# Kernel optimization log

Measured on AMD Instinct MI355X. Metric: run time of the kernel, lower is better.

The kernel has to match this reference:

```python
import jax, jax.numpy as jnp
import numpy as np

OUT, IN = 4096, 4096
PACKED = (OUT * IN + 1) // 2


def setup_inputs() -> dict:
    key = jax.random.key(0)
    k1, k2, k3, k4, k5 = jax.random.split(key, 5)
    x = jax.random.normal(k1, (4, 2048, IN), dtype=jnp.float32)
    weight_packed = jax.random.randint(k2, (PACKED,), 0, 256, dtype=jnp.int32)
    scale = jax.random.uniform(k3, (OUT, 1), dtype=jnp.float32) * 0.01 + 1e-4
    zero_point = jax.random.uniform(k4, (OUT, 1), dtype=jnp.float32) * 8.0
    bias = jax.random.normal(k5, (OUT,), dtype=jnp.float32) * 0.02
    return {"x": x, "weight_packed": weight_packed, "scale": scale,
            "zero_point": zero_point, "bias": bias}


def _dequant_weight(weight_packed, scale, zero_point):
    # Unpack two 4-bit nibbles per byte; low nibble first (matches torch.stack dim=1 + flatten)
    low = (weight_packed & 15).astype(jnp.float32)          # [PACKED]
    high = ((weight_packed >> 4) & 15).astype(jnp.float32)   # [PACKED]
    unpacked = jnp.stack([low, high], axis=1).reshape(-1)     # [2*PACKED]
    w = unpacked[: OUT * IN].reshape(OUT, IN)
    # weight * scale - zero_point * scale == (weight - zero_point) * scale
    return (w - zero_point) * scale                           # [OUT, IN]


def reference(x, weight_packed, scale, zero_point, bias):
    w = _dequant_weight(weight_packed, scale, zero_point)
    # F.linear: x @ w.T + bias
    return jnp.einsum('bsi,oi->bso', x, w) + bias
```

## Files before the change

kernel.cpp:

```cpp
#include <hip/hip_runtime.h>
#include <hip/hip_bf16.h>


typedef __bf16 bf16;
typedef __attribute__((ext_vector_type(8))) __bf16 bf16x8;
typedef __attribute__((ext_vector_type(4))) float f32x4;
typedef __attribute__((ext_vector_type(4))) unsigned int u32x4;

#define OUT_DIM 4096
#define IN_DIM  4096
#define M_DIM   8192

__global__ __launch_bounds__(256) void cvt_x_kernel(
    const float* __restrict__ x, bf16* __restrict__ xb)
{
  const long t = (long)blockIdx.x * 256 + threadIdx.x;
  const long i = t * 8;
  const f32x4 a = *(const f32x4*)(x + i);
  const f32x4 b = *(const f32x4*)(x + i + 4);
  union { bf16 h[8]; u32x4 u; } r;
#pragma unroll
  for (int q = 0; q < 4; ++q) { r.h[q] = (bf16)a[q]; r.h[4+q] = (bf16)b[q]; }
  *(u32x4*)(xb + i) = r.u;
}

__global__ __launch_bounds__(256) void repack_w_kernel(
    const int* __restrict__ wp, unsigned int* __restrict__ wb)
{
  const long t = (long)blockIdx.x * 256 + threadIdx.x;
  const long e = t * 16;
  u32x4 r;
#pragma unroll
  for (int q = 0; q < 4; ++q) {
    const int4 p = *(const int4*)(wp + e + q * 4);
    r[q] = (unsigned)(p.x & 255) | ((unsigned)(p.y & 255) << 8) |
           ((unsigned)(p.z & 255) << 16) | ((unsigned)(p.w & 255) << 24);
  }
  *(u32x4*)(wb + t * 4) = r;
}

__global__ __launch_bounds__(512, 2) void gemm_bt_bias_kernel(
    const bf16* __restrict__ A, const unsigned char* __restrict__ WP,
    const float* __restrict__ scale, const float* __restrict__ zp,
    const float* __restrict__ bias, float* __restrict__ C)
{
  const int N = OUT_DIM, K = IN_DIM;
  const int NT = IN_DIM / 64;

  __shared__ bf16 smA[2][2][256][32];
  __shared__ unsigned int smB[2][2][256][4];

  const int bid = blockIdx.x;
  const int swz = (bid & 7) * (512 / 8) + (bid >> 3);
  const int bm = swz >> 4;
  const int bn = swz & 15;

  const int tid  = threadIdx.x;
  const int wave = tid >> 6;
  const int lane = tid & 63;
  const int wr = wave >> 2;
  const int wc = wave & 3;

  const long row0 = (long)bm * 256;
  const long col0 = (long)bn * 256;

  const int L0 = tid * 16;
  const int L1 = 8192 + tid * 16;
  const int Lw0 = L0 ^ (((L0 >> 9) & 1) << 5);
  const int Lw1 = L1 ^ (((L1 >> 9) & 1) << 5);
  const int sr0 = Lw0 >> 6, sc0 = (Lw0 & 63) >> 1;
  const int sr1 = Lw1 >> 6, sc1 = (Lw1 & 63) >> 1;
  const bf16* a0 = A + (row0 + sr0) * (long)K + sc0;
  const bf16* a1 = A + (row0 + sr1) * (long)K + sc1;

  const int brow  = tid >> 2;
  const int bbyte = (tid & 3) * 4;
  const unsigned char* w0 = WP + (col0 + brow) * 2048L + bbyte;
  const unsigned char* w1 = WP + (col0 + brow + 128) * 2048L + bbyte;

#define STAGE_G(BUF, KS, KOFF) do {                                             \
    char* Ah = (char*)&smA[BUF][KS][0][0];                                      \
    char* Bh = (char*)&smB[BUF][KS][0][0];                                      \
    __builtin_amdgcn_global_load_lds(                                           \
        (const __attribute__((address_space(1))) void*)(a0 + (KOFF)),           \
        (__attribute__((address_space(3))) void*)(Ah + L0), 16, 0, 0);          \
    __builtin_amdgcn_global_load_lds(                                           \
        (const __attribute__((address_space(1))) void*)(a1 + (KOFF)),           \
        (__attribute__((address_space(3))) void*)(Ah + L1), 16, 0, 0);          \
    __builtin_amdgcn_global_load_lds(                                           \
        (const __attribute__((address_space(1))) void*)(w0 + ((KOFF) >> 1)),    \
        (__attribute__((address_space(3))) void*)(Bh + tid * 4), 4, 0, 0);      \
    __builtin_amdgcn_global_load_lds(                                           \
        (const __attribute__((address_space(1))) void*)(w1 + ((KOFF) >> 1)),    \
        (__attribute__((address_space(3))) void*)(Bh + 2048 + tid * 4), 4, 0, 0);\
  } while (0)

  const int lane15 = lane & 15;
  const int rb  = (lane15 * 64 + ((lane >> 4) << 4)) ^ ((lane & 8) << 2);
  const int wrB = wr * 8192;
  const int rBb = (wc * 64 + lane15) * 16 + ((lane >> 4) << 2);

  float sv[4], zv[4];
#pragma unroll
  for (int f = 0; f < 4; ++f) {
    const int n = (int)col0 + wc * 64 + f * 16 + lane15;
    sv[f] = scale[n];
    zv[f] = zp[n] * sv[f];
  }

  f32x4 acc[8][4] = {};

#define PHASE(BUF, KS, STAGE_STMT, VM_STMT) do {                                \
    VM_STMT;                                                                    \
    __builtin_amdgcn_s_barrier();                                               \
    asm volatile("" ::: "memory");        \
    const char* Ab = (const char*)&smA[BUF][KS][0][0];                          \
    const char* Bp = (const char*)&smB[BUF][KS][0][0];                          \
    unsigned int pk[4];                                                         \
    _Pragma("unroll")                                                           \
    for (int f = 0; f < 4; ++f) pk[f] = *(const unsigned int*)(Bp + rBb + f * 256); \
    bf16x8 fa[8];                                                               \
    _Pragma("unroll")                                                           \
    for (int f = 0; f < 8; ++f) fa[f] = *(const bf16x8*)(Ab + wrB + f * 1024 + rb); \
    STAGE_STMT;                                                                 \
    bf16x8 fb[4];                                                               \
    _Pragma("unroll")                                                           \
    for (int f = 0; f < 4; ++f) {                                               \
      const float fs = sv[f], fz = zv[f];                                       \
      _Pragma("unroll")                                                         \
      for (int e = 0; e < 8; ++e)                                               \
        fb[f][e] = (bf16)((float)((pk[f] >> (4 * e)) & 15u) * fs - fz);         \
    }                                                                           \
    __builtin_amdgcn_s_setprio(1);                                              \
    _Pragma("unroll")                                                           \
    for (int i = 0; i < 8; ++i)                                                 \
      _Pragma("unroll")                                                         \
      for (int j = 0; j < 4; ++j)                                               \
        acc[i][j] = __builtin_amdgcn_mfma_f32_16x16x32_bf16(fa[i], fb[j], acc[i][j], 0, 0, 0); \
    __builtin_amdgcn_s_setprio(0);                                              \
  } while (0)

  STAGE_G(0, 0, 0);
  STAGE_G(0, 1, 32);

  for (int T = 0; T < NT; ++T) {
    const int buf = T & 1;
    const int nbuf = buf ^ 1;
    const int nko = (T + 1) * 64;
    const bool st = (T + 1 < NT);

    PHASE(buf, 0,
          { if (st) STAGE_G(nbuf, 0, nko); },
          { asm volatile("s_waitcnt vmcnt(4)" ::: "memory"); });
    PHASE(buf, 1,
          { if (st) STAGE_G(nbuf, 1, nko + 32); },
          { if (T == NT - 1) asm volatile("s_waitcnt vmcnt(0)" ::: "memory");
            else             asm volatile("s_waitcnt vmcnt(4)" ::: "memory"); });
  }

  const long cr0 = row0 + wr * 128 + ((lane >> 4) << 2);
  const long cc0 = col0 + wc * 64 + lane15;
#pragma unroll
  for (int j = 0; j < 4; ++j) {
    const long gc = cc0 + j * 16;
    const float bv = bias[gc];
#pragma unroll
    for (int mf = 0; mf < 8; ++mf) {
      float* cp = C + (cr0 + mf * 16) * (long)N + gc;
#pragma unroll
      for (int r = 0; r < 4; ++r)
        cp[(long)r * N] = acc[mf][j][r] + bv;
    }
  }
#undef PHASE
#undef STAGE_G
}

extern "C" void kernel_launch(void* const* d_in, const int* in_sizes, int n_in,
                              void* d_out, int out_size, void* d_ws, size_t ws_size,
                              hipStream_t stream)
{
  const float* x     = (const float*)d_in[0];
  const int*   wp    = (const int*)d_in[1];
  const float* scale = (const float*)d_in[2];
  const float* zp    = (const float*)d_in[3];
  const float* bias  = (const float*)d_in[4];
  float* out = (float*)d_out;

  bf16* Xb = (bf16*)d_ws;
  unsigned int* Wb = (unsigned int*)((char*)d_ws + 67108864);

  cvt_x_kernel<<<(M_DIM * (long)IN_DIM / 8) / 256, 256, 0, stream>>>(x, Xb);
  repack_w_kernel<<<(OUT_DIM * (long)IN_DIM / 2 / 16) / 256, 256, 0, stream>>>(wp, Wb);
  gemm_bt_bias_kernel<<<512, 512, 0, stream>>>(
      Xb, (const unsigned char*)Wb, scale, zp, bias, out);
}
```

Before: 335.1 us.

## Factor dequant affine into epilogue via row sums and bit-trick nibble to bf16

Each 4-bit weight is turned directly into the bf16 value 1+q/16 by OR-ing the nibble into the mantissa of 1.0. The scale and zero-point are applied once in the epilogue as acc*16s - s(16+z)*rowsum(x) + bias. This removes the per-element int-to-float conversion, multiply and subtract from the MFMA inner loop. The row sums of the bf16-converted activations are computed with wave reductions and atomics in the conversion kernel, which needs an extra memset. The weight LDS layout is also reordered so each lane reads its four packed words with a single 16-byte load. The cost is a subtraction of two large terms in the epilogue, which can lose some precision.

```diff
diff --git a/kernel.cpp b/kernel.cpp
--- a/kernel.cpp
+++ b/kernel.cpp
@@ -12,7 +12,7 @@
 #define M_DIM   8192
 
 __global__ __launch_bounds__(256) void cvt_x_kernel(
-    const float* __restrict__ x, bf16* __restrict__ xb)
+    const float* __restrict__ x, bf16* __restrict__ xb, float* __restrict__ rowsum)
 {
   const long t = (long)blockIdx.x * 256 + threadIdx.x;
   const long i = t * 8;
@@ -22,6 +22,12 @@
 #pragma unroll
   for (int q = 0; q < 4; ++q) { r.h[q] = (bf16)a[q]; r.h[4+q] = (bf16)b[q]; }
   *(u32x4*)(xb + i) = r.u;
+  float p = 0.f;
+#pragma unroll
+  for (int q = 0; q < 8; ++q) p += (float)r.h[q];
+#pragma unroll
+  for (int off = 32; off > 0; off >>= 1) p += __shfl_down(p, off);
+  if ((threadIdx.x & 63) == 0) atomicAdd(&rowsum[(long)(t >> 9)], p);
 }
 
 __global__ __launch_bounds__(256) void repack_w_kernel(
@@ -42,13 +48,14 @@
 __global__ __launch_bounds__(512, 2) void gemm_bt_bias_kernel(
     const bf16* __restrict__ A, const unsigned char* __restrict__ WP,
     const float* __restrict__ scale, const float* __restrict__ zp,
-    const float* __restrict__ bias, float* __restrict__ C)
+    const float* __restrict__ bias, const float* __restrict__ rowsum,
+    float* __restrict__ C)
 {
   const int N = OUT_DIM, K = IN_DIM;
   const int NT = IN_DIM / 64;
 
   __shared__ bf16 smA[2][2][256][32];
-  __shared__ unsigned int smB[2][2][256][4];
+  __shared__ unsigned int smB[2][2][1024];
 
   const int bid = blockIdx.x;
   const int swz = (bid & 7) * (512 / 8) + (bid >> 3);
@@ -56,8 +63,8 @@
   const int bn = swz & 15;
 
   const int tid  = threadIdx.x;
+  const int lane = tid & 63;
   const int wave = tid >> 6;
-  const int lane = tid & 63;
   const int wr = wave >> 2;
   const int wc = wave & 3;
 
@@ -73,14 +80,15 @@
   const bf16* a0 = A + (row0 + sr0) * (long)K + sc0;
   const bf16* a1 = A + (row0 + sr1) * (long)K + sc1;
 
-  const int brow  = tid >> 2;
-  const int bbyte = (tid & 3) * 4;
-  const unsigned char* w0 = WP + (col0 + brow) * 2048L + bbyte;
-  const unsigned char* w1 = WP + (col0 + brow + 128) * 2048L + bbyte;
+  const int W0 = tid, W1 = 512 + tid;
+  const long bn0 = col0 + (W0 >> 8) * 64 + (W0 & 3) * 16 + ((W0 >> 4) & 15);
+  const long bn1 = col0 + (W1 >> 8) * 64 + (W1 & 3) * 16 + ((W1 >> 4) & 15);
+  const unsigned char* w0 = WP + bn0 * 2048L + ((W0 >> 2) & 3) * 4;
+  const unsigned char* w1 = WP + bn1 * 2048L + ((W1 >> 2) & 3) * 4;
 
 #define STAGE_G(BUF, KS, KOFF) do {                                             \
     char* Ah = (char*)&smA[BUF][KS][0][0];                                      \
-    char* Bh = (char*)&smB[BUF][KS][0][0];                                      \
+    char* Bh = (char*)&smB[BUF][KS][0];                                         \
     __builtin_amdgcn_global_load_lds(                                           \
         (const __attribute__((address_space(1))) void*)(a0 + (KOFF)),           \
         (__attribute__((address_space(3))) void*)(Ah + L0), 16, 0, 0);          \
@@ -98,14 +106,15 @@
   const int lane15 = lane & 15;
   const int rb  = (lane15 * 64 + ((lane >> 4) << 4)) ^ ((lane & 8) << 2);
   const int wrB = wr * 8192;
-  const int rBb = (wc * 64 + lane15) * 16 + ((lane >> 4) << 2);
-
-  float sv[4], zv[4];
+  const int rBb = ((wc * 16 + lane15) * 4 + (lane >> 4)) * 16;
+
+  float sv16[4], ev[4];
 #pragma unroll
   for (int f = 0; f < 4; ++f) {
     const int n = (int)col0 + wc * 64 + f * 16 + lane15;
-    sv[f] = scale[n];
-    zv[f] = zp[n] * sv[f];
+    const float s = scale[n];
+    sv16[f] = 16.f * s;
+    ev[f]   = s * (16.f + zp[n]);
   }
 
   f32x4 acc[8][4] = {};
@@ -115,10 +124,8 @@
     __builtin_amdgcn_s_barrier();                                               \
     asm volatile("" ::: "memory");        \
     const char* Ab = (const char*)&smA[BUF][KS][0][0];                          \
-    const char* Bp = (const char*)&smB[BUF][KS][0][0];                          \
-    unsigned int pk[4];                                                         \
-    _Pragma("unroll")                                                           \
-    for (int f = 0; f < 4; ++f) pk[f] = *(const unsigned int*)(Bp + rBb + f * 256); \
+    const char* Bp = (const char*)&smB[BUF][KS][0];                             \
+    const u32x4 pkv = *(const u32x4*)(Bp + rBb);                                \
     bf16x8 fa[8];                                                               \
     _Pragma("unroll")                                                           \
     for (int f = 0; f < 8; ++f) fa[f] = *(const bf16x8*)(Ab + wrB + f * 1024 + rb); \
@@ -126,10 +133,14 @@
     bf16x8 fb[4];                                                               \
     _Pragma("unroll")                                                           \
     for (int f = 0; f < 4; ++f) {                                               \
-      const float fs = sv[f], fz = zv[f];                                       \
+      union { unsigned int u[4]; bf16x8 h; } bb;                                \
+      const unsigned int pk = pkv[f];                                           \
       _Pragma("unroll")                                                         \
-      for (int e = 0; e < 8; ++e)                                               \
-        fb[f][e] = (bf16)((float)((pk[f] >> (4 * e)) & 15u) * fs - fz);         \
+      for (int g = 0; g < 4; ++g) {                                             \
+        const unsigned int tt = pk >> (8 * g);                                  \
+        bb.u[g] = 0x3F803F80u | ((tt & 15u) << 3) | ((tt & 0xF0u) << 15);       \
+      }                                                                         \
+      fb[f] = bb.h;                                                             \
     }                                                                           \
     __builtin_amdgcn_s_setprio(1);                                              \
     _Pragma("unroll")                                                           \
@@ -164,12 +175,14 @@
   for (int j = 0; j < 4; ++j) {
     const long gc = cc0 + j * 16;
     const float bv = bias[gc];
+    const float sj = sv16[j], e = ev[j];
 #pragma unroll
     for (int mf = 0; mf < 8; ++mf) {
-      float* cp = C + (cr0 + mf * 16) * (long)N + gc;
+      const long gr = cr0 + mf * 16;
+      float* cp = C + gr * (long)N + gc;
 #pragma unroll
       for (int r = 0; r < 4; ++r)
-        cp[(long)r * N] = acc[mf][j][r] + bv;
+        cp[(long)r * N] = acc[mf][j][r] * sj - e * rowsum[gr + r] + bv;
     }
   }
 #undef PHASE
@@ -189,9 +202,11 @@
 
   bf16* Xb = (bf16*)d_ws;
   unsigned int* Wb = (unsigned int*)((char*)d_ws + 67108864);
-
-  cvt_x_kernel<<<(M_DIM * (long)IN_DIM / 8) / 256, 256, 0, stream>>>(x, Xb);
+  float* Rs = (float*)((char*)d_ws + 67108864 + 8388608);
+
+  hipMemsetAsync(Rs, 0, M_DIM * sizeof(float), stream);
+  cvt_x_kernel<<<(M_DIM * (long)IN_DIM / 8) / 256, 256, 0, stream>>>(x, Xb, Rs);
   repack_w_kernel<<<(OUT_DIM * (long)IN_DIM / 2 / 16) / 256, 256, 0, stream>>>(wp, Wb);
   gemm_bt_bias_kernel<<<512, 512, 0, stream>>>(
-      Xb, (const unsigned char*)Wb, scale, zp, bias, out);
-}
+      Xb, (const unsigned char*)Wb, scale, zp, bias, Rs, out);
+}
```

New measurement: 310.7 us. 1.08x faster.
